# Kernel optimization log

Measured on AMD Instinct MI355X. Metric: run time of the kernel, lower is better.

Reference implementation:

```python
import jax, jax.numpy as jnp
import numpy as np

N, C, T, V = 16, 128, 128, 25
K, H, OC = 3, 8, 256          # kernel_size subsets, heads, out_channels
HOPMAX = 12                   # hop values in [0, 12); emb_table size HOPMAX
EPS_BN = 1e-5
EPS_NORM = 1e-4


def setup_inputs() -> dict:
    key = jax.random.key(0)
    ks = jax.random.split(key, 12)
    s = 0.05
    x = jax.random.normal(ks[0], (N, C, T, V), jnp.float32)
    hop = jax.random.randint(ks[1], (V, V), 0, HOPMAX)
    emb_table = jax.random.normal(ks[2], (K, H, HOPMAX), jnp.float32) * s
    # A initialized as identity (as in the module) plus small noise for nontrivial grads
    A = jnp.tile(jnp.eye(V, dtype=jnp.float32), (K, H, 1, 1)) \
        + jax.random.normal(ks[3], (K, H, V, V), jnp.float32) * s
    w_block = jax.random.normal(ks[4], (K * OC, C // H), jnp.float32) * s  # grouped 1x1 conv, groups=K*H
    b_block = jax.random.normal(ks[5], (K * OC,), jnp.float32) * s
    bn_gamma = jnp.ones((OC,), jnp.float32)
    bn_beta = jnp.zeros((OC,), jnp.float32)
    res_w = jax.random.normal(ks[6], (OC, C), jnp.float32) * s  # residual 1x1 conv
    res_b = jax.random.normal(ks[7], (OC,), jnp.float32) * s
    res_bn_gamma = jnp.ones((OC,), jnp.float32)
    res_bn_beta = jnp.zeros((OC,), jnp.float32)
    return {"x": x, "hop": hop, "emb_table": emb_table, "A": A,
            "w_block": w_block, "b_block": b_block,
            "bn_gamma": bn_gamma, "bn_beta": bn_beta,
            "res_w": res_w, "res_b": res_b,
            "res_bn_gamma": res_bn_gamma, "res_bn_beta": res_bn_beta}


def _batchnorm(x, gamma, beta):
    # training-mode BatchNorm2d: batch stats over (N, T, V), biased variance
    m = jnp.mean(x, axis=(0, 2, 3), keepdims=True)
    v = jnp.var(x, axis=(0, 2, 3), keepdims=True)
    xn = (x - m) * jax.lax.rsqrt(v + EPS_BN)
    return gamma[None, :, None, None] * xn + beta[None, :, None, None]


def _l2_col_norm(w):
    # torch.norm(w, p=2, dim=-2, keepdim=True) + 1e-4  (in-degree normalization)
    return jnp.sqrt(jnp.sum(w * w, axis=-2, keepdims=True)) + EPS_NORM


def reference(x, hop, emb_table, A, w_block, b_block, bn_gamma, bn_beta,
              res_w, res_b, res_bn_gamma, res_bn_beta):
    n, c, t, v = x.shape
    # residual: 1x1 TemporalConv2d + BN (in_channels != out_channels)
    res = jnp.einsum('nctv,oc->notv', x, res_w) + res_b[None, :, None, None]
    res = _batchnorm(res, res_bn_gamma, res_bn_beta)

    # hop-embedding gather -> [K, H, V, V]; fuse normalized B and A
    B = emb_table[:, :, hop]
    BnA = B / _l2_col_norm(B) + A / _l2_col_norm(A)

    # graph conv: einsum over joint dim v (broadcast over k)
    xh = x.reshape(n, H, c // H, t, v)                      # [N,H,C/H,T,V]
    y = jnp.einsum('nhctv,khvw->nkhctw', xh, BnA)           # [N,K,H,C/H,T,V]
    y = y.reshape(n, K * H, c // H, t, v)                   # groups = K*H

    # grouped 1x1 conv: per-group [C/H -> OC/H] GEMM
    wg = w_block.reshape(K * H, OC // H, c // H)
    out = jnp.einsum('ngctv,goc->ngotv', y, wg)             # [N,K*H,OC/H,T,V]
    out = out.reshape(n, K * OC, t, v) + b_block[None, :, None, None]

    # sum over the K kernel subsets
    out = out.reshape(n, K, OC, t, v).sum(axis=1)
    out = _batchnorm(out, bn_gamma, bn_beta)
    return jax.nn.relu(out + res)
```

## Files before the change

kernel.cpp:

```cpp
#include <hip/hip_runtime.h>
#include <stdint.h>

typedef __attribute__((ext_vector_type(8))) short short8;
typedef __attribute__((ext_vector_type(4))) float f32x4;

#define B_STATS  60416ull
#define B_RESW2  64512ull
#define B_E2     1178624ull
#define B_XB     7994368ull
#define B_MAIN   21625856ull
#define B_RES    47840256ull

#define NTV 51200.0f

__device__ __forceinline__ unsigned short f2bf(float f) {
    unsigned u = __float_as_uint(f);
    return (unsigned short)((u + 0x7fffu + ((u >> 16) & 1u)) >> 16);
}
__device__ __forceinline__ float bf2f(unsigned s) { return __uint_as_float(s << 16); }

__device__ __forceinline__ float wave_sum(float v) {
#pragma unroll
    for (int m = 1; m < 64; m <<= 1) v += __shfl_xor(v, m, 64);
    return v;
}

__device__ __forceinline__ void gl_lds16(const unsigned short* g, unsigned short* l) {
    __builtin_amdgcn_global_load_lds(
        (const __attribute__((address_space(1))) unsigned int*)g,
        (__attribute__((address_space(3))) unsigned int*)l, 16, 0, 0);
}
__device__ __forceinline__ void stage_pair(const unsigned short* g0, const unsigned short* g1,
                                           unsigned short* d) {
    gl_lds16(g0, d);
    gl_lds16(g1, d + 512);
}

__device__ __forceinline__ int swz_idx(int row, int quad) {
    int rowX = row ^ ((row >> 2) & 1);
    return rowX * 32 + ((quad ^ (row & 3)) << 3);
}

__global__ __launch_bounds__(256) void k_prep2x(const int* __restrict__ hop,
                                                const float* __restrict__ emb,
                                                const float* __restrict__ A,
                                                const float* __restrict__ res_w,
                                                const float* __restrict__ w_block,
                                                unsigned short* __restrict__ E2,
                                                const float* __restrict__ x,
                                                unsigned short* __restrict__ xb,
                                                float* __restrict__ stats,
                                                unsigned short* __restrict__ resw2) {
    int bid = blockIdx.x, tid = threadIdx.x;
    if (bid < 128) {
        __shared__ float bl[3*625];
        __shared__ float wl[3*64];
        int half = bid & 1, og = (bid >> 1) & 7, h = bid >> 4;

        if (tid < 75) {
            int k3 = tid / 25, w = tid - k3*25;
            int g = k3*8 + h;
            float nb = 0.f, na = 0.f;
            for (int v = 0; v < 25; v++) {
                float e = emb[g*12 + hop[v*25 + w]];
                nb += e*e;
                float a = A[((size_t)g*25 + v)*25 + w];
                na += a*a;
            }
            nb = sqrtf(nb) + 1e-4f;
            na = sqrtf(na) + 1e-4f;
            for (int v = 0; v < 25; v++) {
                float e = emb[g*12 + hop[v*25 + w]];
                float a = A[((size_t)g*25 + v)*25 + w];
                bl[k3*625 + v*25 + w] = e/nb + a/na;
            }
        }
        if (tid < 192) {
            int k3 = tid >> 6, o = (tid >> 4) & 3, c = tid & 15;
            wl[tid] = w_block[(k3*256 + h*32 + og*4 + o)*16 + c];
        }
        __syncthreads();

        unsigned short* dst = E2 + (size_t)(h*8 + og)*53248;
        int e0 = half * 26624;
        for (int e = e0 + tid; e < e0 + 26624; e += 256) {
            int kc = e >> 12;
            int n  = (e >> 5) & 127;
            int kk = e & 31;
            int k  = kc*32 + kk;
            int o  = n >> 5, w = n & 31;
            float val = 0.f;
            if (k < 400 && w < 25) {
                int c = k / 25, v = k - c*25;
                val = wl[0*64 + o*16 + c] * bl[0*625 + v*25 + w]
                    + wl[1*64 + o*16 + c] * bl[1*625 + v*25 + w]
                    + wl[2*64 + o*16 + c] * bl[2*625 + v*25 + w];
            }
            dst[e] = f2bf(val);
        }
    } else if (bid < 2176) {
        int b = bid - 128;
        int n_ = b >> 7, t_ = b & 127;
        unsigned short* row = xb + (size_t)b * 3328;
        for (int idx = tid; idx < 3200; idx += 256) {
            int c = idx / 25, v = idx - c*25;
            float val = x[(((size_t)n_*128 + c)*128 + t_)*25 + v];
            row[(c >> 4)*416 + (c & 15)*25 + v] = f2bf(val);
        }
        if (tid < 128) row[(tid >> 4)*416 + 400 + (tid & 15)] = 0;
    } else if (bid == 2176) {
#pragma unroll
        for (int i = 0; i < 4; i++) stats[i*256 + tid] = 0.f;
    } else {
        int base = (bid - 2177) * 4096 + tid * 16;
#pragma unroll
        for (int j = 0; j < 16; j++) resw2[base + j] = f2bf(res_w[base + j]);
    }
}

__global__ __launch_bounds__(256) void k_mm(const unsigned short* __restrict__ xb,
                                            const unsigned short* __restrict__ E2,
                                            unsigned short* __restrict__ mainp,
                                            const float* __restrict__ x,
                                            const unsigned short* __restrict__ resw2,
                                            unsigned short* __restrict__ resp,
                                            float* __restrict__ stats) {
    __shared__ unsigned short lds[16384];
    int bid = blockIdx.x, tid = threadIdx.x;
    int lane = tid & 63, wave = tid >> 6;
    int wm = wave >> 1, wn = wave & 1;
    int lane15 = lane & 15, quad = lane >> 4;

    int Lrow0 = wave*32 + (lane >> 2), Lq = lane & 3;
    int r0 = Lrow0 ^ ((Lrow0 >> 2) & 1), q0 = Lq ^ (r0 & 3);
    int Lrow1 = Lrow0 + 16;
    int r1 = Lrow1 ^ ((Lrow1 >> 2) & 1), q1 = Lq ^ (r1 & 3);
    const int adoff = wave*1024 + lane*8;

    if (bid < 1024) {
        int h = bid & 7, og = (bid >> 3) & 7, mt = bid >> 6;

        const unsigned short* agA0 = xb + (size_t)(mt*128 + r0)*3328 + h*416 + q0*8;
        const unsigned short* agA1 = xb + (size_t)(mt*128 + r1)*3328 + h*416 + q1*8;
        const unsigned short* eb   = E2 + (size_t)(h*8 + og)*53248;
        const unsigned short* bgB0 = eb + r0*32 + q0*8;
        const unsigned short* bgB1 = eb + r1*32 + q1*8;

        f32x4 acc[4][4] = {};

        stage_pair(agA0,        agA1,        lds + adoff);
        stage_pair(bgB0,        bgB1,        lds + 4096 + adoff);
        stage_pair(agA0 + 32,   agA1 + 32,   lds + 8192 + adoff);
        stage_pair(bgB0 + 4096, bgB1 + 4096, lds + 8192 + 4096 + adoff);

        for (int kc = 0; kc < 13; kc++) {
            if (kc < 12) asm volatile("s_waitcnt vmcnt(4)" ::: "memory");
            else         asm volatile("s_waitcnt vmcnt(0)" ::: "memory");
            __builtin_amdgcn_s_barrier();

            int cur = (kc & 1) << 13;
            const unsigned short* Ac = lds + cur;
            const unsigned short* Bc = lds + cur + 4096;
            short8 af[4], bq[4];
#pragma unroll
            for (int i = 0; i < 4; i++) {
                af[i] = *(const short8*)&Ac[swz_idx(wm*64 + i*16 + lane15, quad)];
                bq[i] = *(const short8*)&Bc[swz_idx(wn*64 + i*16 + lane15, quad)];
            }
            asm volatile("s_waitcnt lgkmcnt(0)" ::: "memory");
            __builtin_amdgcn_sched_barrier(0);
            __builtin_amdgcn_s_barrier();

            if (kc < 11) {
                stage_pair(agA0 + (kc+2)*32,           agA1 + (kc+2)*32,
                           lds + cur + adoff);
                stage_pair(bgB0 + (size_t)(kc+2)*4096, bgB1 + (size_t)(kc+2)*4096,
                           lds + cur + 4096 + adoff);
                __builtin_amdgcn_sched_barrier(0);
            }
#pragma unroll
            for (int i = 0; i < 4; i++)
#pragma unroll
                for (int j = 0; j < 4; j++)
                    acc[i][j] = __builtin_amdgcn_mfma_f32_16x16x32_bf16(af[i], bq[j], acc[i][j], 0, 0, 0);
        }

        float s1[2] = {0.f, 0.f}, s2[2] = {0.f, 0.f};
#pragma unroll
        for (int j = 0; j < 4; j++) {
            int w = (j & 1)*16 + lane15;
            int p = j >> 1;
            if (w < 25) {
                int oc = h*32 + og*4 + wn*2 + p;
#pragma unroll
                for (int i = 0; i < 4; i++) {
                    int tb = wm*64 + i*16 + quad*4;
#pragma unroll
                    for (int r = 0; r < 4; r++) {
                        float val = acc[i][j][r];
                        mainp[((size_t)(mt*256 + oc)*128 + tb + r)*25 + w] = f2bf(val);
                        s1[p] += val;
                        s2[p] = fmaf(val, val, s2[p]);
                    }
                }
            }
        }
#pragma unroll
        for (int p = 0; p < 2; p++) {
            float a = wave_sum(s1[p]);
            float b = wave_sum(s2[p]);
            if (lane == 0) {
                int oc = h*32 + og*4 + wn*2 + p;
                atomicAdd(&stats[oc], a);
                atomicAdd(&stats[256 + oc], b);
            }
        }
    } else {
        int b2 = bid - 1024;
        int nt = (b2 >= 400) ? 1 : 0;
        int mt = b2 - nt*400;

        int n  = mt / 25;
        int off = (mt - n*25) * 128;
        const float* xb2 = x + (size_t)n*409600 + off;

        int c2 = tid >> 4, seg = tid & 15;

        const unsigned short* rb0 = resw2 + (size_t)(nt*128 + r0)*128 + q0*8;
        const unsigned short* rb1 = resw2 + (size_t)(nt*128 + r1)*128 + q1*8;

        f32x4 acc[4][4] = {};

        for (int kc = 0; kc < 4; kc++) {
            stage_pair(rb0 + kc*32, rb1 + kc*32, lds + 4096 + adoff);
            const float* xc0 = xb2 + (size_t)(kc*32 + 2*c2)*3200;
            const float* xc1 = xc0 + 3200;
            int wbase = 2*(c2 & 3), qn = c2 >> 2;
#pragma unroll
            for (int j = 0; j < 8; j++) {
                int m = seg + 16*j;
                unsigned pk = (unsigned)f2bf(xc0[m]) | ((unsigned)f2bf(xc1[m]) << 16);
                *(unsigned*)&lds[swz_idx(m, qn) + wbase] = pk;
            }
            __syncthreads();

            short8 af[4], bq[4];
#pragma unroll
            for (int i = 0; i < 4; i++) {
                af[i] = *(const short8*)&lds[swz_idx(wm*64 + i*16 + lane15, quad)];
                bq[i] = *(const short8*)&lds[4096 + swz_idx(wn*64 + i*16 + lane15, quad)];
            }
#pragma unroll
            for (int i = 0; i < 4; i++)
#pragma unroll
                for (int j = 0; j < 4; j++)
                    acc[i][j] = __builtin_amdgcn_mfma_f32_16x16x32_bf16(af[i], bq[j], acc[i][j], 0, 0, 0);
            __syncthreads();
        }

#pragma unroll
        for (int j = 0; j < 4; j++) {
            int oc = nt*128 + wn*64 + j*16 + lane15;
            float s1 = 0.f, s2 = 0.f;
#pragma unroll
            for (int i = 0; i < 4; i++) {
                int m2b = mt*128 + wm*64 + i*16 + quad*4;
#pragma unroll
                for (int r = 0; r < 4; r++) {
                    float val = acc[i][j][r];
                    int m2e = m2b + r;
                    int b = m2e / 25, v = m2e - b*25;
                    int nn = b >> 7, t = b & 127;
                    resp[((size_t)(nn*256 + oc)*128 + t)*25 + v] = f2bf(val);
                    s1 += val;
                    s2 = fmaf(val, val, s2);
                }
            }
            s1 += __shfl_xor(s1, 16, 64); s1 += __shfl_xor(s1, 32, 64);
            s2 += __shfl_xor(s2, 16, 64); s2 += __shfl_xor(s2, 32, 64);
            if (quad == 0) {
                atomicAdd(&stats[512 + oc], s1);
                atomicAdd(&stats[768 + oc], s2);
            }
        }
    }
}

__global__ __launch_bounds__(256) void k_final(const float* __restrict__ bn_g,
                                               const float* __restrict__ bn_b,
                                               const float* __restrict__ rbn_g,
                                               const float* __restrict__ rbn_b,
                                               const float* __restrict__ stats,
                                               const unsigned short* __restrict__ mainp,
                                               const unsigned short* __restrict__ resp,
                                               float* __restrict__ out) {
    __shared__ float4 cf[8];
    int bid = blockIdx.x, tid = threadIdx.x;
    int base_row = (bid * 1024) / 400;
    if (tid < 8) {
        int row = base_row + tid;
        if (row < 4096) {
            int oc = row & 255;
            const float inv = 1.f / NTV;
            float s1 = stats[oc],       s2 = stats[256 + oc];
            float r1v = stats[512 + oc], r2v = stats[768 + oc];
            float mm = s1*inv, vm = s2*inv - mm*mm;
            float mr = r1v*inv, vr = r2v*inv - mr*mr;
            float a1 = bn_g[oc]  * rsqrtf(vm + 1e-5f);
            float c1 = bn_b[oc]  - a1*mm;
            float a2 = rbn_g[oc] * rsqrtf(vr + 1e-5f);
            float c2 = rbn_b[oc] - a2*mr;
            cf[tid] = make_float4(a1, c1, a2, c2);
        }
    }
    __syncthreads();

    const uint4* m4 = (const uint4*)mainp;
    const uint4* r4 = (const uint4*)resp;
    float4* o4 = (float4*)out;
#pragma unroll
    for (int r = 0; r < 4; r++) {
        int chunk = bid*1024 + r*256 + tid;
        uint4 mu = m4[chunk];
        uint4 ru = r4[chunk];
        float4 C = cf[chunk/400 - base_row];
        float4 f0, f1;
        f0.x = fmaxf(fmaf(C.x, __uint_as_float(mu.x << 16),        C.y)
                   + fmaf(C.z, __uint_as_float(ru.x << 16),        C.w), 0.f);
        f0.y = fmaxf(fmaf(C.x, __uint_as_float(mu.x & 0xffff0000u), C.y)
                   + fmaf(C.z, __uint_as_float(ru.x & 0xffff0000u), C.w), 0.f);
        f0.z = fmaxf(fmaf(C.x, __uint_as_float(mu.y << 16),        C.y)
                   + fmaf(C.z, __uint_as_float(ru.y << 16),        C.w), 0.f);
        f0.w = fmaxf(fmaf(C.x, __uint_as_float(mu.y & 0xffff0000u), C.y)
                   + fmaf(C.z, __uint_as_float(ru.y & 0xffff0000u), C.w), 0.f);
        f1.x = fmaxf(fmaf(C.x, __uint_as_float(mu.z << 16),        C.y)
                   + fmaf(C.z, __uint_as_float(ru.z << 16),        C.w), 0.f);
        f1.y = fmaxf(fmaf(C.x, __uint_as_float(mu.z & 0xffff0000u), C.y)
                   + fmaf(C.z, __uint_as_float(ru.z & 0xffff0000u), C.w), 0.f);
        f1.z = fmaxf(fmaf(C.x, __uint_as_float(mu.w << 16),        C.y)
                   + fmaf(C.z, __uint_as_float(ru.w << 16),        C.w), 0.f);
        f1.w = fmaxf(fmaf(C.x, __uint_as_float(mu.w & 0xffff0000u), C.y)
                   + fmaf(C.z, __uint_as_float(ru.w & 0xffff0000u), C.w), 0.f);
        o4[chunk*2]     = f0;
        o4[chunk*2 + 1] = f1;
    }
}

extern "C" void kernel_launch(void* const* d_in, const int* in_sizes, int n_in,
                              void* d_out, int out_size, void* d_ws, size_t ws_size,
                              hipStream_t stream) {
    const float* x        = (const float*)d_in[0];
    const int*   hop      = (const int*)  d_in[1];
    const float* emb      = (const float*)d_in[2];
    const float* A        = (const float*)d_in[3];
    const float* w_block  = (const float*)d_in[4];
    const float* bn_g     = (const float*)d_in[6];
    const float* bn_b     = (const float*)d_in[7];
    const float* res_w    = (const float*)d_in[8];
    const float* rbn_g    = (const float*)d_in[10];
    const float* rbn_b    = (const float*)d_in[11];
    float* out = (float*)d_out;

    char* ws = (char*)d_ws;
    float*          stats  = (float*)(ws + B_STATS);
    unsigned short* resw2  = (unsigned short*)(ws + B_RESW2);
    unsigned short* E2     = (unsigned short*)(ws + B_E2);
    unsigned short* xb     = (unsigned short*)(ws + B_XB);
    unsigned short* mainp  = (unsigned short*)(ws + B_MAIN);
    unsigned short* resp   = (unsigned short*)(ws + B_RES);

    k_prep2x <<<2185, 256, 0, stream>>>(hop, emb, A, res_w, w_block, E2, x, xb, stats, resw2);
    k_mm     <<<1824, 256, 0, stream>>>(xb, E2, mainp, x, resw2, resp, stats);
    k_final  <<<1600, 256, 0, stream>>>(bn_g, bn_b, rbn_g, rbn_b, stats, mainp, resp, out);
}
```

Baseline: 216.5 us.

## Move residual GEMM into prep kernel, split graph-conv GEMM into own kernel

The residual 1x1-conv GEMM moves from the matmul kernel into the prep kernel, where it runs alongside the E2 build and x bf16 conversion. It converts res_w to bf16 on the fly instead of reading a pre-converted copy, and stats zeroing becomes a hipMemsetAsync. The graph-conv GEMM becomes its own kernel with a simpler single-stage-ahead double buffer that uses __syncthreads instead of manual vmcnt waits. The goal is better load balance and an earlier start for the residual work, at the cost of an extra memset launch and a possibly weaker software pipeline in the main GEMM.

New measurement: 209.9 us. 1.03x faster.

```diff
diff --git a/kernel.cpp b/kernel.cpp
--- a/kernel.cpp
+++ b/kernel.cpp
@@ -5,7 +5,6 @@
 typedef __attribute__((ext_vector_type(4))) float f32x4;
 
 #define B_STATS  60416ull
-#define B_RESW2  64512ull
 #define B_E2     1178624ull
 #define B_XB     7994368ull
 #define B_MAIN   21625856ull
@@ -49,12 +48,14 @@
                                                 unsigned short* __restrict__ E2,
                                                 const float* __restrict__ x,
                                                 unsigned short* __restrict__ xb,
-                                                float* __restrict__ stats,
-                                                unsigned short* __restrict__ resw2) {
+                                                unsigned short* __restrict__ resp,
+                                                float* __restrict__ stats) {
+    __shared__ __align__(16) char smem[16384];
     int bid = blockIdx.x, tid = threadIdx.x;
+
     if (bid < 128) {
-        __shared__ float bl[3*625];
-        __shared__ float wl[3*64];
+        float* bl = (float*)smem;
+        float* wl = (float*)smem + 1875;
         int half = bid & 1, og = (bid >> 1) & 7, h = bid >> 4;
 
         if (tid < 75) {
@@ -98,149 +99,38 @@
             }
             dst[e] = f2bf(val);
         }
-    } else if (bid < 2176) {
-        int b = bid - 128;
-        int n_ = b >> 7, t_ = b & 127;
-        unsigned short* row = xb + (size_t)b * 3328;
-        for (int idx = tid; idx < 3200; idx += 256) {
-            int c = idx / 25, v = idx - c*25;
-            float val = x[(((size_t)n_*128 + c)*128 + t_)*25 + v];
-            row[(c >> 4)*416 + (c & 15)*25 + v] = f2bf(val);
-        }
-        if (tid < 128) row[(tid >> 4)*416 + 400 + (tid & 15)] = 0;
-    } else if (bid == 2176) {
-#pragma unroll
-        for (int i = 0; i < 4; i++) stats[i*256 + tid] = 0.f;
-    } else {
-        int base = (bid - 2177) * 4096 + tid * 16;
-#pragma unroll
-        for (int j = 0; j < 16; j++) resw2[base + j] = f2bf(res_w[base + j]);
-    }
-}
-
-__global__ __launch_bounds__(256) void k_mm(const unsigned short* __restrict__ xb,
-                                            const unsigned short* __restrict__ E2,
-                                            unsigned short* __restrict__ mainp,
-                                            const float* __restrict__ x,
-                                            const unsigned short* __restrict__ resw2,
-                                            unsigned short* __restrict__ resp,
-                                            float* __restrict__ stats) {
-    __shared__ unsigned short lds[16384];
-    int bid = blockIdx.x, tid = threadIdx.x;
-    int lane = tid & 63, wave = tid >> 6;
-    int wm = wave >> 1, wn = wave & 1;
-    int lane15 = lane & 15, quad = lane >> 4;
-
-    int Lrow0 = wave*32 + (lane >> 2), Lq = lane & 3;
-    int r0 = Lrow0 ^ ((Lrow0 >> 2) & 1), q0 = Lq ^ (r0 & 3);
-    int Lrow1 = Lrow0 + 16;
-    int r1 = Lrow1 ^ ((Lrow1 >> 2) & 1), q1 = Lq ^ (r1 & 3);
-    const int adoff = wave*1024 + lane*8;
-
-    if (bid < 1024) {
-        int h = bid & 7, og = (bid >> 3) & 7, mt = bid >> 6;
-
-        const unsigned short* agA0 = xb + (size_t)(mt*128 + r0)*3328 + h*416 + q0*8;
-        const unsigned short* agA1 = xb + (size_t)(mt*128 + r1)*3328 + h*416 + q1*8;
-        const unsigned short* eb   = E2 + (size_t)(h*8 + og)*53248;
-        const unsigned short* bgB0 = eb + r0*32 + q0*8;
-        const unsigned short* bgB1 = eb + r1*32 + q1*8;
-
-        f32x4 acc[4][4] = {};
-
-        stage_pair(agA0,        agA1,        lds + adoff);
-        stage_pair(bgB0,        bgB1,        lds + 4096 + adoff);
-        stage_pair(agA0 + 32,   agA1 + 32,   lds + 8192 + adoff);
-        stage_pair(bgB0 + 4096, bgB1 + 4096, lds + 8192 + 4096 + adoff);
-
-        for (int kc = 0; kc < 13; kc++) {
-            if (kc < 12) asm volatile("s_waitcnt vmcnt(4)" ::: "memory");
-            else         asm volatile("s_waitcnt vmcnt(0)" ::: "memory");
-            __builtin_amdgcn_s_barrier();
-
-            int cur = (kc & 1) << 13;
-            const unsigned short* Ac = lds + cur;
-            const unsigned short* Bc = lds + cur + 4096;
-            short8 af[4], bq[4];
-#pragma unroll
-            for (int i = 0; i < 4; i++) {
-                af[i] = *(const short8*)&Ac[swz_idx(wm*64 + i*16 + lane15, quad)];
-                bq[i] = *(const short8*)&Bc[swz_idx(wn*64 + i*16 + lane15, quad)];
-            }
-            asm volatile("s_waitcnt lgkmcnt(0)" ::: "memory");
-            __builtin_amdgcn_sched_barrier(0);
-            __builtin_amdgcn_s_barrier();
-
-            if (kc < 11) {
-                stage_pair(agA0 + (kc+2)*32,           agA1 + (kc+2)*32,
-                           lds + cur + adoff);
-                stage_pair(bgB0 + (size_t)(kc+2)*4096, bgB1 + (size_t)(kc+2)*4096,
-                           lds + cur + 4096 + adoff);
-                __builtin_amdgcn_sched_barrier(0);
-            }
-#pragma unroll
-            for (int i = 0; i < 4; i++)
-#pragma unroll
-                for (int j = 0; j < 4; j++)
-                    acc[i][j] = __builtin_amdgcn_mfma_f32_16x16x32_bf16(af[i], bq[j], acc[i][j], 0, 0, 0);
-        }
-
-        float s1[2] = {0.f, 0.f}, s2[2] = {0.f, 0.f};
-#pragma unroll
-        for (int j = 0; j < 4; j++) {
-            int w = (j & 1)*16 + lane15;
-            int p = j >> 1;
-            if (w < 25) {
-                int oc = h*32 + og*4 + wn*2 + p;
-#pragma unroll
-                for (int i = 0; i < 4; i++) {
-                    int tb = wm*64 + i*16 + quad*4;
-#pragma unroll
-                    for (int r = 0; r < 4; r++) {
-                        float val = acc[i][j][r];
-                        mainp[((size_t)(mt*256 + oc)*128 + tb + r)*25 + w] = f2bf(val);
-                        s1[p] += val;
-                        s2[p] = fmaf(val, val, s2[p]);
-                    }
-                }
-            }
-        }
-#pragma unroll
-        for (int p = 0; p < 2; p++) {
-            float a = wave_sum(s1[p]);
-            float b = wave_sum(s2[p]);
-            if (lane == 0) {
-                int oc = h*32 + og*4 + wn*2 + p;
-                atomicAdd(&stats[oc], a);
-                atomicAdd(&stats[256 + oc], b);
-            }
-        }
-    } else {
-        int b2 = bid - 1024;
+    } else if (bid < 928) {
+        unsigned short* lds = (unsigned short*)smem;
+        int b2 = bid - 128;
         int nt = (b2 >= 400) ? 1 : 0;
         int mt = b2 - nt*400;
+
+        int lane = tid & 63, wave = tid >> 6;
+        int wm = wave >> 1, wn = wave & 1;
+        int lane15 = lane & 15, quad = lane >> 4;
 
         int n  = mt / 25;
         int off = (mt - n*25) * 128;
         const float* xb2 = x + (size_t)n*409600 + off;
+        const float* rw  = res_w + (size_t)nt*128*128;
 
         int c2 = tid >> 4, seg = tid & 15;
-
-        const unsigned short* rb0 = resw2 + (size_t)(nt*128 + r0)*128 + q0*8;
-        const unsigned short* rb1 = resw2 + (size_t)(nt*128 + r1)*128 + q1*8;
+        int wbase = 2*(c2 & 3), qn = c2 >> 2;
 
         f32x4 acc[4][4] = {};
 
         for (int kc = 0; kc < 4; kc++) {
-            stage_pair(rb0 + kc*32, rb1 + kc*32, lds + 4096 + adoff);
             const float* xc0 = xb2 + (size_t)(kc*32 + 2*c2)*3200;
             const float* xc1 = xc0 + 3200;
-            int wbase = 2*(c2 & 3), qn = c2 >> 2;
+            const float2* rp2 = (const float2*)(rw + kc*32 + 2*c2);
 #pragma unroll
             for (int j = 0; j < 8; j++) {
                 int m = seg + 16*j;
-                unsigned pk = (unsigned)f2bf(xc0[m]) | ((unsigned)f2bf(xc1[m]) << 16);
-                *(unsigned*)&lds[swz_idx(m, qn) + wbase] = pk;
+                unsigned pkA = (unsigned)f2bf(xc0[m]) | ((unsigned)f2bf(xc1[m]) << 16);
+                *(unsigned*)&lds[swz_idx(m, qn) + wbase] = pkA;
+                float2 rv = rp2[m*64];
+                unsigned pkB = (unsigned)f2bf(rv.x) | ((unsigned)f2bf(rv.y) << 16);
+                *(unsigned*)&lds[4096 + swz_idx(m, qn) + wbase] = pkB;
             }
             __syncthreads();
 
@@ -282,6 +172,103 @@
                 atomicAdd(&stats[512 + oc], s1);
                 atomicAdd(&stats[768 + oc], s2);
             }
+        }
+    } else {
+        int b = bid - 928;
+        int n_ = b >> 7, t_ = b & 127;
+        unsigned short* row = xb + (size_t)b * 3328;
+        for (int idx = tid; idx < 3200; idx += 256) {
+            int c = idx / 25, v = idx - c*25;
+            float val = x[(((size_t)n_*128 + c)*128 + t_)*25 + v];
+            row[(c >> 4)*416 + (c & 15)*25 + v] = f2bf(val);
+        }
+        if (tid < 128) row[(tid >> 4)*416 + 400 + (tid & 15)] = 0;
+    }
+}
+
+__global__ __launch_bounds__(256) void k_gc(const unsigned short* __restrict__ xb,
+                                            const unsigned short* __restrict__ E2,
+                                            unsigned short* __restrict__ mainp,
+                                            float* __restrict__ stats) {
+    __shared__ unsigned short lds[16384];
+    int bid = blockIdx.x, tid = threadIdx.x;
+    int lane = tid & 63, wave = tid >> 6;
+    int wm = wave >> 1, wn = wave & 1;
+    int lane15 = lane & 15, quad = lane >> 4;
+
+    int Lrow0 = wave*32 + (lane >> 2), Lq = lane & 3;
+    int r0 = Lrow0 ^ ((Lrow0 >> 2) & 1), q0 = Lq ^ (r0 & 3);
+    int Lrow1 = Lrow0 + 16;
+    int r1 = Lrow1 ^ ((Lrow1 >> 2) & 1), q1 = Lq ^ (r1 & 3);
+    const int adoff = wave*1024 + lane*8;
+
+    int h = bid & 7, og = (bid >> 3) & 7, mt = bid >> 6;
+
+    const unsigned short* agA0 = xb + (size_t)(mt*128 + r0)*3328 + h*416 + q0*8;
+    const unsigned short* agA1 = xb + (size_t)(mt*128 + r1)*3328 + h*416 + q1*8;
+    const unsigned short* eb   = E2 + (size_t)(h*8 + og)*53248;
+    const unsigned short* bgB0 = eb + r0*32 + q0*8;
+    const unsigned short* bgB1 = eb + r1*32 + q1*8;
+
+    f32x4 acc[4][4] = {};
+
+    stage_pair(agA0, agA1, lds + adoff);
+    stage_pair(bgB0, bgB1, lds + 4096 + adoff);
+    __syncthreads();
+
+    for (int kc = 0; kc < 13; kc++) {
+        int cur = (kc & 1) << 13;
+        if (kc < 12) {
+            int nxt = 8192 - cur;
+            stage_pair(agA0 + (kc+1)*32,           agA1 + (kc+1)*32,           lds + nxt + adoff);
+            stage_pair(bgB0 + (size_t)(kc+1)*4096, bgB1 + (size_t)(kc+1)*4096, lds + nxt + 4096 + adoff);
+            __builtin_amdgcn_sched_barrier(0);
+        }
+        const unsigned short* Ac = lds + cur;
+        const unsigned short* Bc = lds + cur + 4096;
+
+        short8 af[4], bq[4];
+#pragma unroll
+        for (int i = 0; i < 4; i++) {
+            af[i] = *(const short8*)&Ac[swz_idx(wm*64 + i*16 + lane15, quad)];
+            bq[i] = *(const short8*)&Bc[swz_idx(wn*64 + i*16 + lane15, quad)];
+        }
+#pragma unroll
+        for (int i = 0; i < 4; i++)
+#pragma unroll
+            for (int j = 0; j < 4; j++)
+                acc[i][j] = __builtin_amdgcn_mfma_f32_16x16x32_bf16(af[i], bq[j], acc[i][j], 0, 0, 0);
+        if (kc < 12) __syncthreads();
+    }
+
+    float s1[2] = {0.f, 0.f}, s2[2] = {0.f, 0.f};
+#pragma unroll
+    for (int j = 0; j < 4; j++) {
+        int w = (j & 1)*16 + lane15;
+        int p = j >> 1;
+        if (w < 25) {
+            int oc = h*32 + og*4 + wn*2 + p;
+#pragma unroll
+            for (int i = 0; i < 4; i++) {
+                int tb = wm*64 + i*16 + quad*4;
+#pragma unroll
+                for (int r = 0; r < 4; r++) {
+                    float val = acc[i][j][r];
+                    mainp[((size_t)(mt*256 + oc)*128 + tb + r)*25 + w] = f2bf(val);
+                    s1[p] += val;
+                    s2[p] = fmaf(val, val, s2[p]);
+                }
+            }
+        }
+    }
+#pragma unroll
+    for (int p = 0; p < 2; p++) {
+        float a = wave_sum(s1[p]);
+        float b = wave_sum(s2[p]);
+        if (lane == 0) {
+            int oc = h*32 + og*4 + wn*2 + p;
+            atomicAdd(&stats[oc], a);
+            atomicAdd(&stats[256 + oc], b);
         }
     }
 }
@@ -363,13 +350,13 @@
 
     char* ws = (char*)d_ws;
     float*          stats  = (float*)(ws + B_STATS);
-    unsigned short* resw2  = (unsigned short*)(ws + B_RESW2);
     unsigned short* E2     = (unsigned short*)(ws + B_E2);
     unsigned short* xb     = (unsigned short*)(ws + B_XB);
     unsigned short* mainp  = (unsigned short*)(ws + B_MAIN);
     unsigned short* resp   = (unsigned short*)(ws + B_RES);
 
-    k_prep2x <<<2185, 256, 0, stream>>>(hop, emb, A, res_w, w_block, E2, x, xb, stats, resw2);
-    k_mm     <<<1824, 256, 0, stream>>>(xb, E2, mainp, x, resw2, resp, stats);
+    hipMemsetAsync(stats, 0, 4096, stream);
+    k_prep2x <<<2976, 256, 0, stream>>>(hop, emb, A, res_w, w_block, E2, x, xb, resp, stats);
+    k_gc     <<<1024, 256, 0, stream>>>(xb, E2, mainp, stats);
     k_final  <<<1600, 256, 0, stream>>>(bn_g, bn_b, rbn_g, rbn_b, stats, mainp, resp, out);
 }
```
